# Performance work log

Hardware: AMD Instinct MI355X
Metric: run time of the kernel (lower is better)

## Reference

```python
import jax, jax.numpy as jnp
import numpy as np
from jax import lax

H = 64  # hidden size for all 4 layers

def _run_layer(inp, Wi, Wh, bi, bh):
    # inp: [B, T, D_in]; Wi: [H, D_in]; Wh: [H, H]; bi, bh: [H]
    # PyTorch RNN cell: h_t = tanh(x_t @ Wi^T + bi + h_{t-1} @ Wh^T + bh)
    pre = jnp.einsum('btd,hd->bth', inp, Wi) + (bi + bh)  # input part, batched GEMM
    B = inp.shape[0]
    h0 = jnp.zeros((B, H), dtype=inp.dtype)

    def step(h, x_t):
        h_new = jnp.tanh(x_t + h @ Wh.T)
        return h_new, h_new

    _, ys = lax.scan(step, h0, pre.transpose(1, 0, 2))  # scan over time
    return ys.transpose(1, 0, 2)  # [B, T, H]


def setup_inputs() -> dict:
    key = jax.random.key(0)
    ks = jax.random.split(key, 12)
    B, T, D_in = 512, 1024, 52
    s_in = 1.0 / np.sqrt(H)  # PyTorch RNN init scale U(-1/sqrt(H), 1/sqrt(H))
    u = lambda k, shape: jax.random.uniform(k, shape, jnp.float32, -s_in, s_in)
    return {
        'x': jax.random.normal(ks[0], (B, T, D_in), jnp.float32),
        'Wih0': u(ks[1], (H, D_in)),
        'Whh0': u(ks[2], (H, H)),
        'bih0': u(ks[3], (H,)),
        'bhh0': u(ks[4], (H,)),
        'Wih': u(ks[5], (3, H, H)),   # layers 1..3 input weights
        'Whh': u(ks[6], (3, H, H)),
        'bih': u(ks[7], (3, H)),
        'bhh': u(ks[8], (3, H)),
        'Wfc': u(ks[9], (64, H)),     # fc: Linear(64, output_dims=64)
        'bfc': u(ks[10], (64,)),
    }


def reference(x, Wih0, Whh0, bih0, bhh0, Wih, Whh, bih, bhh, Wfc, bfc):
    h = _run_layer(x, Wih0, Whh0, bih0, bhh0)
    for l in range(3):  # fixed small layer loop
        h = _run_layer(h, Wih[l], Whh[l], bih[l], bhh[l])
    y = jnp.einsum('bth,oh->bto', h, Wfc) + bfc
    return y
```

## Files before the change

kernel.cpp:

```cpp
#include <hip/hip_runtime.h>


typedef __fp16 h2 __attribute__((ext_vector_type(2)));

__device__ __forceinline__ h2 pk2(float a, float b) {
#if __has_builtin(__builtin_amdgcn_cvt_pkrtz)
  return __builtin_amdgcn_cvt_pkrtz(a, b);
#else
  h2 r; r.x = (__fp16)a; r.y = (__fp16)b; return r;
#endif
}

__device__ __forceinline__ float fdot2f(h2 a, h2 b, float c) {
#if __has_builtin(__builtin_amdgcn_fdot2)
  return __builtin_amdgcn_fdot2(a, b, c, false);
#else
  return c + (float)a.x * (float)b.x + (float)a.y * (float)b.y;
#endif
}

__device__ __forceinline__ h2 bc(unsigned int u) {
  return __builtin_bit_cast(h2, u);
}

__device__ __forceinline__ float fast_tanh(float x) {
  float e = __expf(2.0f * x);
#if __has_builtin(__builtin_amdgcn_rcpf)
  return 1.0f - 2.0f * __builtin_amdgcn_rcpf(e + 1.0f);
#else
  return 1.0f - 2.0f / (e + 1.0f);
#endif
}

#define T_STEPS 1024

#define ACC(U, J)                                         \
  do {                                                    \
    h2 hv_ = bc(U);                                       \
    if ((J) < 26) {                                       \
      if ((J) & 1) a1 = fdot2f(hv_, w[(J)], a1);          \
      else         a0 = fdot2f(hv_, w[(J)], a0);          \
    } else {                                              \
      if ((J) & 1) c1 = fdot2f(hv_, w[(J) - 26], c1);     \
      else         c0 = fdot2f(hv_, w[(J) - 26], c0);     \
    }                                                     \
  } while (0)

__global__ __launch_bounds__(256) void pre0_kernel(
    const float* __restrict__ x, const float* __restrict__ Wih0,
    const float* __restrict__ bih0, const float* __restrict__ bhh0,
    unsigned int* __restrict__ pre0p) {
  __shared__ unsigned int xsh[64 * 26];
  __shared__ unsigned int wsh[64 * 26];
  const int tid  = threadIdx.x;
  const int lane = tid & 63;
  const int wv   = tid >> 6;

  const float4* xg = (const float4*)(x + (long)blockIdx.x * 64 * 52);
  const float4* wg = (const float4*)Wih0;
#pragma unroll
  for (int i = 0; i < 4; ++i) {
    int idx = tid + i * 256;
    if (idx < 832) {
      float4 v = xg[idx];
      xsh[idx * 2]     = __builtin_bit_cast(unsigned int, pk2(v.x, v.y));
      xsh[idx * 2 + 1] = __builtin_bit_cast(unsigned int, pk2(v.z, v.w));
      float4 u = wg[idx];
      wsh[idx * 2]     = __builtin_bit_cast(unsigned int, pk2(u.x, u.y));
      wsh[idx * 2 + 1] = __builtin_bit_cast(unsigned int, pk2(u.z, u.w));
    }
  }
  const float bias = bih0[lane] + bhh0[lane];
  __syncthreads();

  h2 w[26];
  {
    const uint2* wr2 = (const uint2*)(wsh + lane * 26);
#pragma unroll
    for (int k = 0; k < 13; ++k) {
      uint2 u = wr2[k];
      w[2 * k]     = bc(u.x);
      w[2 * k + 1] = bc(u.y);
    }
  }

  const long pbase = (long)blockIdx.x * 32;
#pragma unroll 1
  for (int rp = wv * 8; rp < wv * 8 + 8; ++rp) {
    const uint4* xp = (const uint4*)(xsh + rp * 52);
    float a0 = bias, a1 = 0.f, c0 = bias, c1 = 0.f;
#pragma unroll
    for (int q = 0; q < 13; ++q) {
      uint4 v = xp[q];
      ACC(v.x, 4 * q + 0);
      ACC(v.y, 4 * q + 1);
      ACC(v.z, 4 * q + 2);
      ACC(v.w, 4 * q + 3);
    }
    pre0p[(pbase + rp) * 64 + lane] =
        __builtin_bit_cast(unsigned int, pk2(a0 + a1, c0 + c1));
  }
}

#define GEMV64(RES, HPTR, INIT)                               \
  do {                                                        \
    const uint4* hp_ = (const uint4*)(HPTR);                  \
    float a0_ = (INIT), a1_ = 0.f, a2_ = 0.f, a3_ = 0.f;      \
    _Pragma("unroll")                                         \
    for (int q_ = 0; q_ < 8; ++q_) {                          \
      uint4 u_ = hp_[q_];                                     \
      a0_ = fdot2f(bc(u_.x), w[4 * q_ + 0], a0_);             \
      a1_ = fdot2f(bc(u_.y), w[4 * q_ + 1], a1_);             \
      a2_ = fdot2f(bc(u_.z), w[4 * q_ + 2], a2_);             \
      a3_ = fdot2f(bc(u_.w), w[4 * q_ + 3], a3_);             \
    }                                                         \
    RES = (a0_ + a1_) + (a2_ + a3_);                          \
  } while (0)

__global__ __launch_bounds__(512, 4) void rnn_pipe(
    const unsigned int* __restrict__ pre0p, const float* __restrict__ Whh0,
    const float* __restrict__ Wih, const float* __restrict__ Whh,
    const float* __restrict__ bih, const float* __restrict__ bhh,
    const float* __restrict__ Wfc, const float* __restrict__ bfc,
    float* __restrict__ out) {
  const int tid  = threadIdx.x;
  const int lane = tid & 63;
  const int wv   = __builtin_amdgcn_readfirstlane(tid >> 6);
  const int b    = blockIdx.x;

  __shared__ __attribute__((aligned(16))) __fp16 hbuf[4][2][4][64];
  __shared__ float Pbuf[3][2][4][64];

  ((float*)hbuf)[tid]       = 0.f;
  ((float*)hbuf)[tid + 512] = 0.f;

  const float* W;
  float bias = 0.f;
  int role, L;
  if (wv == 7) {
    role = 2; L = 3; W = Wfc; bias = bfc[lane];
  } else if ((wv & 1) == 0) {
    role = 0; L = wv >> 1;
    W = (L == 0) ? Whh0 : (Whh + (L - 1) * 4096);
    if (L > 0) bias = bih[(L - 1) * 64 + lane] + bhh[(L - 1) * 64 + lane];
  } else {
    role = 1; L = (wv + 1) >> 1;
    W = Wih + (L - 1) * 4096;
  }

  h2 w[32];
  const float2* wsrc = (const float2*)(W + lane * 64);
#pragma unroll
  for (int k = 0; k < 32; ++k) {
    float2 v = wsrc[k];
    w[k] = pk2(v.x, v.y);
  }

  const long rowbase = (long)b * T_STEPS;
  const unsigned int* pp = pre0p + (long)b * 512 * 64 + lane;
  float* op = out + rowbase * 64 + lane;

  unsigned int pc0 = 0, pc1 = 0;
  if (wv == 0) { pc0 = pp[0]; pc1 = pp[64]; }

  __syncthreads();

#pragma unroll 1
  for (int k = 0; k < 256 + 7; ++k) {
    const unsigned kk = (unsigned)(k - wv);
    const int rd = (k - 1) & 1;
    const int wr = k & 1;
    if (kk < 256u) {
      if (role == 0) {
        float p0_, p1_, p2_, p3_;
        if (L == 0) {
          h2 u0 = bc(pc0), u1 = bc(pc1);
          p0_ = (float)u0.x; p1_ = (float)u0.y;
          p2_ = (float)u1.x; p3_ = (float)u1.y;
          pp += 128;
          if (kk + 1 < 256u) { pc0 = pp[0]; pc1 = pp[64]; }
        } else {
          p0_ = Pbuf[L - 1][rd][0][lane];
          p1_ = Pbuf[L - 1][rd][1][lane];
          p2_ = Pbuf[L - 1][rd][2][lane];
          p3_ = Pbuf[L - 1][rd][3][lane];
        }
        float hv;
        GEMV64(hv, hbuf[L][rd][3], bias);
        float h0v = fast_tanh(hv + p0_);
        hbuf[L][wr][0][lane] = (__fp16)h0v;
        GEMV64(hv, hbuf[L][wr][0], bias);
        float h1v = fast_tanh(hv + p1_);
        hbuf[L][wr][1][lane] = (__fp16)h1v;
        GEMV64(hv, hbuf[L][wr][1], bias);
        float h2v = fast_tanh(hv + p2_);
        hbuf[L][wr][2][lane] = (__fp16)h2v;
        GEMV64(hv, hbuf[L][wr][2], bias);
        float h3v = fast_tanh(hv + p3_);
        hbuf[L][wr][3][lane] = (__fp16)h3v;
      } else if (role == 1) {
        float q0, q1, q2, q3;
        GEMV64(q0, hbuf[L - 1][rd][0], 0.f);
        GEMV64(q1, hbuf[L - 1][rd][1], 0.f);
        GEMV64(q2, hbuf[L - 1][rd][2], 0.f);
        GEMV64(q3, hbuf[L - 1][rd][3], 0.f);
        Pbuf[L - 1][wr][0][lane] = q0;
        Pbuf[L - 1][wr][1][lane] = q1;
        Pbuf[L - 1][wr][2][lane] = q2;
        Pbuf[L - 1][wr][3][lane] = q3;
      } else {
        float q0, q1, q2, q3;
        GEMV64(q0, hbuf[3][rd][0], bias);
        GEMV64(q1, hbuf[3][rd][1], bias);
        GEMV64(q2, hbuf[3][rd][2], bias);
        GEMV64(q3, hbuf[3][rd][3], bias);
        op[0]   = q0;
        op[64]  = q1;
        op[128] = q2;
        op[192] = q3;
        op += 256;
      }
    }
    __syncthreads();
  }
}

extern "C" void kernel_launch(void* const* d_in, const int* in_sizes, int n_in,
                              void* d_out, int out_size, void* d_ws,
                              size_t ws_size, hipStream_t stream) {
  const float* x    = (const float*)d_in[0];
  const float* Wih0 = (const float*)d_in[1];
  const float* Whh0 = (const float*)d_in[2];
  const float* bih0 = (const float*)d_in[3];
  const float* bhh0 = (const float*)d_in[4];
  const float* Wih  = (const float*)d_in[5];
  const float* Whh  = (const float*)d_in[6];
  const float* bih  = (const float*)d_in[7];
  const float* bhh  = (const float*)d_in[8];
  const float* Wfc  = (const float*)d_in[9];
  const float* bfc  = (const float*)d_in[10];
  float* out = (float*)d_out;

  const int B = in_sizes[0] / (T_STEPS * 52);
  const int R = B * T_STEPS;

  unsigned int* pre0p = (unsigned int*)d_ws;

  pre0_kernel<<<R / 64, 256, 0, stream>>>(x, Wih0, bih0, bhh0, pre0p);
  rnn_pipe<<<B, 512, 0, stream>>>(pre0p, Whh0, Wih, Whh, bih, bhh, Wfc, bfc,
                                  out);
}
```

Baseline: 674.3 us.

## Fuse layer-0 input projection into the pipelined RNN kernel

Removes the separate pre0 kernel and its fp16 workspace round-trip. Wave 1 (the otherwise-idle layer-1 input-projection wave) now also streams x rows from global memory, converts them to fp16 in shared memory, and computes the layer-0 input projection one pipeline stage ahead. This saves a kernel launch and the global write and read of the precomputed projections. In exchange, wave 1 does extra work each step, which may lengthen the per-step critical path that every wave waits on at the barrier.

```diff
diff --git a/kernel.cpp b/kernel.cpp
--- a/kernel.cpp
+++ b/kernel.cpp
@@ -21,6 +21,10 @@
 
 __device__ __forceinline__ h2 bc(unsigned int u) {
   return __builtin_bit_cast(h2, u);
+}
+
+__device__ __forceinline__ unsigned int ubc(h2 v) {
+  return __builtin_bit_cast(unsigned int, v);
 }
 
 __device__ __forceinline__ float fast_tanh(float x) {
@@ -33,74 +37,6 @@
 }
 
 #define T_STEPS 1024
-
-#define ACC(U, J)                                         \
-  do {                                                    \
-    h2 hv_ = bc(U);                                       \
-    if ((J) < 26) {                                       \
-      if ((J) & 1) a1 = fdot2f(hv_, w[(J)], a1);          \
-      else         a0 = fdot2f(hv_, w[(J)], a0);          \
-    } else {                                              \
-      if ((J) & 1) c1 = fdot2f(hv_, w[(J) - 26], c1);     \
-      else         c0 = fdot2f(hv_, w[(J) - 26], c0);     \
-    }                                                     \
-  } while (0)
-
-__global__ __launch_bounds__(256) void pre0_kernel(
-    const float* __restrict__ x, const float* __restrict__ Wih0,
-    const float* __restrict__ bih0, const float* __restrict__ bhh0,
-    unsigned int* __restrict__ pre0p) {
-  __shared__ unsigned int xsh[64 * 26];
-  __shared__ unsigned int wsh[64 * 26];
-  const int tid  = threadIdx.x;
-  const int lane = tid & 63;
-  const int wv   = tid >> 6;
-
-  const float4* xg = (const float4*)(x + (long)blockIdx.x * 64 * 52);
-  const float4* wg = (const float4*)Wih0;
-#pragma unroll
-  for (int i = 0; i < 4; ++i) {
-    int idx = tid + i * 256;
-    if (idx < 832) {
-      float4 v = xg[idx];
-      xsh[idx * 2]     = __builtin_bit_cast(unsigned int, pk2(v.x, v.y));
-      xsh[idx * 2 + 1] = __builtin_bit_cast(unsigned int, pk2(v.z, v.w));
-      float4 u = wg[idx];
-      wsh[idx * 2]     = __builtin_bit_cast(unsigned int, pk2(u.x, u.y));
-      wsh[idx * 2 + 1] = __builtin_bit_cast(unsigned int, pk2(u.z, u.w));
-    }
-  }
-  const float bias = bih0[lane] + bhh0[lane];
-  __syncthreads();
-
-  h2 w[26];
-  {
-    const uint2* wr2 = (const uint2*)(wsh + lane * 26);
-#pragma unroll
-    for (int k = 0; k < 13; ++k) {
-      uint2 u = wr2[k];
-      w[2 * k]     = bc(u.x);
-      w[2 * k + 1] = bc(u.y);
-    }
-  }
-
-  const long pbase = (long)blockIdx.x * 32;
-#pragma unroll 1
-  for (int rp = wv * 8; rp < wv * 8 + 8; ++rp) {
-    const uint4* xp = (const uint4*)(xsh + rp * 52);
-    float a0 = bias, a1 = 0.f, c0 = bias, c1 = 0.f;
-#pragma unroll
-    for (int q = 0; q < 13; ++q) {
-      uint4 v = xp[q];
-      ACC(v.x, 4 * q + 0);
-      ACC(v.y, 4 * q + 1);
-      ACC(v.z, 4 * q + 2);
-      ACC(v.w, 4 * q + 3);
-    }
-    pre0p[(pbase + rp) * 64 + lane] =
-        __builtin_bit_cast(unsigned int, pk2(a0 + a1, c0 + c1));
-  }
-}
 
 #define GEMV64(RES, HPTR, INIT)                               \
   do {                                                        \
@@ -117,19 +53,36 @@
     RES = (a0_ + a1_) + (a2_ + a3_);                          \
   } while (0)
 
-__global__ __launch_bounds__(512, 4) void rnn_pipe(
-    const unsigned int* __restrict__ pre0p, const float* __restrict__ Whh0,
-    const float* __restrict__ Wih, const float* __restrict__ Whh,
-    const float* __restrict__ bih, const float* __restrict__ bhh,
-    const float* __restrict__ Wfc, const float* __restrict__ bfc,
-    float* __restrict__ out) {
+#define PREGEMV(RES, XPTR)                                    \
+  do {                                                        \
+    const uint4* xp_ = (const uint4*)(XPTR);                  \
+    float a0_ = bias0, a1_ = 0.f, a2_ = 0.f, a3_ = 0.f;       \
+    _Pragma("unroll")                                         \
+    for (int q_ = 0; q_ < 7; ++q_) {                          \
+      uint4 u_ = xp_[q_];                                     \
+      a0_ = fdot2f(bc(u_.x), w0[4 * q_ + 0], a0_);            \
+      a1_ = fdot2f(bc(u_.y), w0[4 * q_ + 1], a1_);            \
+      a2_ = fdot2f(bc(u_.z), w0[4 * q_ + 2], a2_);            \
+      a3_ = fdot2f(bc(u_.w), w0[4 * q_ + 3], a3_);            \
+    }                                                         \
+    RES = (a0_ + a1_) + (a2_ + a3_);                          \
+  } while (0)
+
+__global__ __launch_bounds__(512, 4) void rnn_fused(
+    const float* __restrict__ x, const float* __restrict__ Wih0,
+    const float* __restrict__ bih0, const float* __restrict__ bhh0,
+    const float* __restrict__ Whh0, const float* __restrict__ Wih,
+    const float* __restrict__ Whh, const float* __restrict__ bih,
+    const float* __restrict__ bhh, const float* __restrict__ Wfc,
+    const float* __restrict__ bfc, float* __restrict__ out) {
   const int tid  = threadIdx.x;
   const int lane = tid & 63;
   const int wv   = __builtin_amdgcn_readfirstlane(tid >> 6);
   const int b    = blockIdx.x;
 
   __shared__ __attribute__((aligned(16))) __fp16 hbuf[4][2][4][64];
-  __shared__ float Pbuf[3][2][4][64];
+  __shared__ __attribute__((aligned(16))) float PB[4][2][4][64];
+  __shared__ __attribute__((aligned(16))) unsigned int pxs[2][4][28];
 
   ((float*)hbuf)[tid]       = 0.f;
   ((float*)hbuf)[tid + 512] = 0.f;
@@ -149,21 +102,57 @@
   }
 
   h2 w[32];
-  const float2* wsrc = (const float2*)(W + lane * 64);
+  {
+    const float2* wsrc = (const float2*)(W + lane * 64);
 #pragma unroll
-  for (int k = 0; k < 32; ++k) {
-    float2 v = wsrc[k];
-    w[k] = pk2(v.x, v.y);
-  }
-
-  const long rowbase = (long)b * T_STEPS;
-  const unsigned int* pp = pre0p + (long)b * 512 * 64 + lane;
-  float* op = out + rowbase * 64 + lane;
-
-  unsigned int pc0 = 0, pc1 = 0;
-  if (wv == 0) { pc0 = pp[0]; pc1 = pp[64]; }
-
+    for (int k = 0; k < 32; ++k) {
+      float2 v = wsrc[k];
+      w[k] = pk2(v.x, v.y);
+    }
+  }
+
+  h2 w0[28];
+  float bias0 = 0.f;
+  float4 xr = {0.f, 0.f, 0.f, 0.f};
+  const float4* xg = (const float4*)(x + (long)b * T_STEPS * 52);
+  const int xrow = (lane / 13) & 3;
+  const int xcol = lane % 13;
+  const bool xact = (lane < 52);
+
+  if (wv == 1) {
+    const float2* w2 = (const float2*)(Wih0 + lane * 52);
+#pragma unroll
+    for (int k = 0; k < 26; ++k) {
+      float2 v = w2[k];
+      w0[k] = pk2(v.x, v.y);
+    }
+    w0[26] = pk2(0.f, 0.f);
+    w0[27] = pk2(0.f, 0.f);
+    bias0 = bih0[lane] + bhh0[lane];
+    if (lane < 16) pxs[lane >> 3][(lane >> 1) & 3][26 + (lane & 1)] = 0u;
+    float4 xa = {0.f, 0.f, 0.f, 0.f}, xb = {0.f, 0.f, 0.f, 0.f};
+    if (xact) {
+      xa = xg[0 * 52 + lane];
+      xb = xg[1 * 52 + lane];
+      xr = xg[2 * 52 + lane];
+      pxs[0][xrow][2 * xcol]     = ubc(pk2(xa.x, xa.y));
+      pxs[0][xrow][2 * xcol + 1] = ubc(pk2(xa.z, xa.w));
+      pxs[1][xrow][2 * xcol]     = ubc(pk2(xb.x, xb.y));
+      pxs[1][xrow][2 * xcol + 1] = ubc(pk2(xb.z, xb.w));
+    }
+  }
   __syncthreads();
+
+  if (wv == 1) {
+    float pv;
+    PREGEMV(pv, pxs[0][0]); PB[0][1][0][lane] = pv;
+    PREGEMV(pv, pxs[0][1]); PB[0][1][1][lane] = pv;
+    PREGEMV(pv, pxs[0][2]); PB[0][1][2][lane] = pv;
+    PREGEMV(pv, pxs[0][3]); PB[0][1][3][lane] = pv;
+  }
+  __syncthreads();
+
+  float* op = out + (long)b * T_STEPS * 64 + lane;
 
 #pragma unroll 1
   for (int k = 0; k < 256 + 7; ++k) {
@@ -172,19 +161,10 @@
     const int wr = k & 1;
     if (kk < 256u) {
       if (role == 0) {
-        float p0_, p1_, p2_, p3_;
-        if (L == 0) {
-          h2 u0 = bc(pc0), u1 = bc(pc1);
-          p0_ = (float)u0.x; p1_ = (float)u0.y;
-          p2_ = (float)u1.x; p3_ = (float)u1.y;
-          pp += 128;
-          if (kk + 1 < 256u) { pc0 = pp[0]; pc1 = pp[64]; }
-        } else {
-          p0_ = Pbuf[L - 1][rd][0][lane];
-          p1_ = Pbuf[L - 1][rd][1][lane];
-          p2_ = Pbuf[L - 1][rd][2][lane];
-          p3_ = Pbuf[L - 1][rd][3][lane];
-        }
+        float p0_ = PB[L][rd][0][lane];
+        float p1_ = PB[L][rd][1][lane];
+        float p2_ = PB[L][rd][2][lane];
+        float p3_ = PB[L][rd][3][lane];
         float hv;
         GEMV64(hv, hbuf[L][rd][3], bias);
         float h0v = fast_tanh(hv + p0_);
@@ -204,10 +184,10 @@
         GEMV64(q1, hbuf[L - 1][rd][1], 0.f);
         GEMV64(q2, hbuf[L - 1][rd][2], 0.f);
         GEMV64(q3, hbuf[L - 1][rd][3], 0.f);
-        Pbuf[L - 1][wr][0][lane] = q0;
-        Pbuf[L - 1][wr][1][lane] = q1;
-        Pbuf[L - 1][wr][2][lane] = q2;
-        Pbuf[L - 1][wr][3][lane] = q3;
+        PB[L][wr][0][lane] = q0;
+        PB[L][wr][1][lane] = q1;
+        PB[L][wr][2][lane] = q2;
+        PB[L][wr][3][lane] = q3;
       } else {
         float q0, q1, q2, q3;
         GEMV64(q0, hbuf[3][rd][0], bias);
@@ -219,6 +199,22 @@
         op[128] = q2;
         op[192] = q3;
         op += 256;
+      }
+    }
+    if (wv == 1) {
+      if (k <= 254) {
+        const unsigned int* xsrc = &pxs[(k + 1) & 1][0][0];
+        float pv;
+        PREGEMV(pv, xsrc + 0 * 28); PB[0][wr][0][lane] = pv;
+        PREGEMV(pv, xsrc + 1 * 28); PB[0][wr][1][lane] = pv;
+        PREGEMV(pv, xsrc + 2 * 28); PB[0][wr][2][lane] = pv;
+        PREGEMV(pv, xsrc + 3 * 28); PB[0][wr][3][lane] = pv;
+      }
+      if (k <= 253 && xact) {
+        float4 xw = xr;
+        if (k <= 252) xr = xg[(k + 3) * 52 + lane];
+        pxs[k & 1][xrow][2 * xcol]     = ubc(pk2(xw.x, xw.y));
+        pxs[k & 1][xrow][2 * xcol + 1] = ubc(pk2(xw.z, xw.w));
       }
     }
     __syncthreads();
@@ -242,11 +238,8 @@
   float* out = (float*)d_out;
 
   const int B = in_sizes[0] / (T_STEPS * 52);
-  const int R = B * T_STEPS;
-
-  unsigned int* pre0p = (unsigned int*)d_ws;
-
-  pre0_kernel<<<R / 64, 256, 0, stream>>>(x, Wih0, bih0, bhh0, pre0p);
-  rnn_pipe<<<B, 512, 0, stream>>>(pre0p, Whh0, Wih, Whh, bih, bhh, Wfc, bfc,
-                                  out);
-}
+  (void)d_ws; (void)ws_size;
+
+  rnn_fused<<<B, 512, 0, stream>>>(x, Wih0, bih0, bhh0, Whh0, Wih, Whh, bih,
+                                   bhh, Wfc, bfc, out);
+}
```

Measured after the change: 815.1 us. 1.21x slower.
